# Kernel tuning notes

Hardware: AMD Instinct MI355X
Metric: run time of the kernel (lower is better)

Reference implementation:

```python
import jax, jax.numpy as jnp
import numpy as np

N = 100000   # nodes
E = 400000   # edges (avg degree 4, NoC-mesh-like)
H = 512      # hidden_channels
F_IN = 1     # num_node_features


def _lin(key, fan_in, fan_out):
    # torch.nn.Linear default init: U(-1/sqrt(fan_in), 1/sqrt(fan_in))
    bound = 1.0 / np.sqrt(fan_in)
    return jax.random.uniform(key, (fan_in, fan_out), jnp.float32, -bound, bound)


def setup_inputs() -> dict:
    key = jax.random.key(0)
    ks = jax.random.split(key, 16)
    inp = {
        "x": jax.random.normal(ks[0], (N, F_IN), jnp.float32),
        "edge_index": jax.random.randint(ks[1], (2, E), 0, N, jnp.int32),
        # conv1: in=1 -> out=512
        "w_rel1": _lin(ks[2], F_IN, H),
        "b_rel1": jax.random.uniform(ks[3], (H,), jnp.float32, -1.0, 1.0),
        "w_root1": _lin(ks[4], F_IN, H),
        # conv2..4: 512 -> 512
        "w_rel2": _lin(ks[5], H, H),
        "b_rel2": jax.random.uniform(ks[6], (H,), jnp.float32, -1/np.sqrt(H), 1/np.sqrt(H)),
        "w_root2": _lin(ks[7], H, H),
        "w_rel3": _lin(ks[8], H, H),
        "b_rel3": jax.random.uniform(ks[9], (H,), jnp.float32, -1/np.sqrt(H), 1/np.sqrt(H)),
        "w_root3": _lin(ks[10], H, H),
        "w_rel4": _lin(ks[11], H, H),
        "b_rel4": jax.random.uniform(ks[12], (H,), jnp.float32, -1/np.sqrt(H), 1/np.sqrt(H)),
        "w_root4": _lin(ks[13], H, H),
    }
    return inp


def _graph_conv(x, src, dst, w_rel, b_rel, w_root):
    # PyG GraphConv (aggr='add'): out_i = W_rel @ sum_{j in N(i)} x_j + b_rel + W_root @ x_i
    # messages flow src (edge_index[0]) -> dst (edge_index[1])
    agg = jax.ops.segment_sum(x[src], dst, num_segments=N)  # [N, F_in]
    return agg @ w_rel + b_rel + x @ w_root


def reference(x, edge_index,
              w_rel1, b_rel1, w_root1,
              w_rel2, b_rel2, w_root2,
              w_rel3, b_rel3, w_root3,
              w_rel4, b_rel4, w_root4):
    src, dst = edge_index[0], edge_index[1]
    x1 = jax.nn.relu(_graph_conv(x,  src, dst, w_rel1, b_rel1, w_root1))
    x2 = jax.nn.relu(_graph_conv(x1, src, dst, w_rel2, b_rel2, w_root2)) + x1
    x3 = _graph_conv(x2, src, dst, w_rel3, b_rel3, w_root3) + x2
    x4 = _graph_conv(x3, src, dst, w_rel4, b_rel4, w_root4) + x3
    return x4
```

## Files before the change

### kernel.cpp

```cpp
#include <hip/hip_runtime.h>

#define NN 100000
#define EE 400000
#define HH 512
#define NB_SCAN 98

typedef __attribute__((ext_vector_type(8))) short short8;
typedef __attribute__((ext_vector_type(8))) unsigned short ushort8;
typedef __attribute__((ext_vector_type(4))) float f32x4;

__device__ inline unsigned short f2b(float f) {
    unsigned int u = __float_as_uint(f);
    return (unsigned short)((u + 0x7fffu + ((u >> 16) & 1u)) >> 16);
}
__device__ inline float b2f(unsigned short b) {
    return __uint_as_float(((unsigned int)b) << 16);
}

__global__ void histo_deg(const int* __restrict__ dst, int* __restrict__ deg) {
    int e = blockIdx.x * blockDim.x + threadIdx.x;
    if (e < EE) atomicAdd(&deg[dst[e]], 1);
}

__global__ void scan_reduce(const int* __restrict__ deg, int* __restrict__ blockSums) {
    __shared__ int s[256];
    int b = blockIdx.x, t = threadIdx.x;
    int base = b * 1024 + t * 4;
    int v = 0;
    #pragma unroll
    for (int j = 0; j < 4; ++j) { int i = base + j; if (i < NN) v += deg[i]; }
    s[t] = v; __syncthreads();
    for (int off = 128; off > 0; off >>= 1) {
        if (t < off) s[t] += s[t + off];
        __syncthreads();
    }
    if (t == 0) blockSums[b] = s[0];
}

__global__ void scan_top(int* __restrict__ blockSums, int* __restrict__ start) {
    __shared__ int s[128];
    int t = threadIdx.x;
    s[t] = (t < NB_SCAN) ? blockSums[t] : 0;
    __syncthreads();
    for (int off = 1; off < 128; off <<= 1) {
        int u = (t >= off) ? s[t - off] : 0;
        __syncthreads();
        s[t] += u;
        __syncthreads();
    }
    if (t < NB_SCAN) blockSums[t] = (t == 0) ? 0 : s[t - 1];
    if (t == 0) start[NN] = EE;
}

__global__ void scan_down(const int* __restrict__ deg, const int* __restrict__ blockSums,
                          int* __restrict__ start, int* __restrict__ cursor) {
    __shared__ int s[256];
    int b = blockIdx.x, t = threadIdx.x;
    int base = b * 1024 + t * 4;
    int v[4]; int sum = 0;
    #pragma unroll
    for (int j = 0; j < 4; ++j) {
        int i = base + j;
        v[j] = (i < NN) ? deg[i] : 0;
        sum += v[j];
    }
    s[t] = sum; __syncthreads();
    for (int off = 1; off < 256; off <<= 1) {
        int u = (t >= off) ? s[t - off] : 0;
        __syncthreads();
        s[t] += u;
        __syncthreads();
    }
    int excl = blockSums[b] + ((t == 0) ? 0 : s[t - 1]);
    #pragma unroll
    for (int j = 0; j < 4; ++j) {
        int i = base + j;
        if (i < NN) { start[i] = excl; cursor[i] = excl; excl += v[j]; }
    }
}

__global__ void csr_fill(const int* __restrict__ src, const int* __restrict__ dst,
                         int* __restrict__ cursor, int* __restrict__ eidx) {
    int e = blockIdx.x * blockDim.x + threadIdx.x;
    if (e < EE) {
        int p = atomicAdd(&cursor[dst[e]], 1);
        eidx[p] = src[e];
    }
}

__global__ void w_transpose_all(
    const float* __restrict__ w0, const float* __restrict__ w1,
    const float* __restrict__ w2, const float* __restrict__ w3,
    const float* __restrict__ w4, const float* __restrict__ w5,
    unsigned short* __restrict__ wt)
{
    int m = blockIdx.x >> 10;
    int idx = ((blockIdx.x & 1023) << 8) + threadIdx.x;
    int n = idx >> 9, k = idx & 511;
    const float* w = (m == 0) ? w0 : (m == 1) ? w1 : (m == 2) ? w2
                   : (m == 3) ? w3 : (m == 4) ? w4 : w5;
    wt[(size_t)m * 262144 + idx] = f2b(w[(size_t)k * HH + n]);
}

__global__ __launch_bounds__(256) void gather_rows_b(
    const unsigned short* __restrict__ xb, const int* __restrict__ start,
    const int* __restrict__ eidx, unsigned short* __restrict__ agg)
{
    int node = blockIdx.x * 4 + (threadIdx.x >> 6);
    if (node >= NN) return;
    int c0 = (threadIdx.x & 63) << 3;
    float a[8] = {0.f,0.f,0.f,0.f,0.f,0.f,0.f,0.f};
    int e0 = start[node], e1 = start[node + 1];
    int e = e0;
    for (; e + 4 <= e1; e += 4) {
        int s0 = eidx[e], s1 = eidx[e + 1], s2 = eidx[e + 2], s3 = eidx[e + 3];
        ushort8 v0 = *(const ushort8*)(xb + (size_t)s0 * HH + c0);
        ushort8 v1 = *(const ushort8*)(xb + (size_t)s1 * HH + c0);
        ushort8 v2 = *(const ushort8*)(xb + (size_t)s2 * HH + c0);
        ushort8 v3 = *(const ushort8*)(xb + (size_t)s3 * HH + c0);
        #pragma unroll
        for (int j = 0; j < 8; ++j)
            a[j] += (b2f(v0[j]) + b2f(v1[j])) + (b2f(v2[j]) + b2f(v3[j]));
    }
    for (; e < e1; ++e) {
        ushort8 v = *(const ushort8*)(xb + (size_t)eidx[e] * HH + c0);
        #pragma unroll
        for (int j = 0; j < 8; ++j) a[j] += b2f(v[j]);
    }
    ushort8 o;
    #pragma unroll
    for (int j = 0; j < 8; ++j) o[j] = f2b(a[j]);
    *(ushort8*)(agg + (size_t)node * HH + c0) = o;
}

__global__ void gather_scalar(const float* __restrict__ x, const int* __restrict__ start,
                              const int* __restrict__ eidx, float* __restrict__ agg0) {
    int i = blockIdx.x * blockDim.x + threadIdx.x;
    if (i >= NN) return;
    float s = 0.f;
    int e1 = start[i + 1];
    for (int e = start[i]; e < e1; ++e) s += x[eidx[e]];
    agg0[i] = s;
}

__global__ void layer1_expand(const float* __restrict__ x,
                              const float* __restrict__ agg0,
                              const float* __restrict__ w_rel,
                              const float* __restrict__ b,
                              const float* __restrict__ w_root,
                              unsigned short* __restrict__ x1b) {
    int idx = blockIdx.x * blockDim.x + threadIdx.x;
    int i = idx >> 7;
    if (i >= NN) return;
    int q = (idx & 127) << 2;
    float a = agg0[i], xv = x[i];
    float4 wr = *(const float4*)&w_rel[q];
    float4 bb = *(const float4*)&b[q];
    float4 wt = *(const float4*)&w_root[q];
    float4 o;
    o.x = fmaxf(fmaf(a, wr.x, fmaf(xv, wt.x, bb.x)), 0.f);
    o.y = fmaxf(fmaf(a, wr.y, fmaf(xv, wt.y, bb.y)), 0.f);
    o.z = fmaxf(fmaf(a, wr.z, fmaf(xv, wt.z, bb.z)), 0.f);
    o.w = fmaxf(fmaf(a, wr.w, fmaf(xv, wt.w, bb.w)), 0.f);
    ushort4 ob = { f2b(o.x), f2b(o.y), f2b(o.z), f2b(o.w) };
    *(ushort4*)&x1b[(size_t)i * HH + q] = ob;
}

__device__ inline void gload16(const void* g, void* l) {
    __builtin_amdgcn_global_load_lds(
        (const __attribute__((address_space(1))) unsigned int*)g,
        (__attribute__((address_space(3))) unsigned int*)l,
        16, 0, 0);
}

template<bool RELU, bool F32OUT>
__global__ __launch_bounds__(256, 3) void gemm_mfma(
    const unsigned short* __restrict__ AB, const unsigned short* __restrict__ XBp,
    const unsigned short* __restrict__ WrT, const unsigned short* __restrict__ WoT,
    const float* __restrict__ bias, const unsigned short* __restrict__ residb,
    float* __restrict__ out, unsigned short* __restrict__ outb)
{
    __shared__ unsigned short As[2 * 128 * 32];
    __shared__ unsigned short Bs[2 * 128 * 32];
    const int tid  = threadIdx.x;
    const int wave = tid >> 6, lane = tid & 63;

    const int bid = blockIdx.x;
    const int nid = (bid & 7) * 391 + (bid >> 3);
    const int col0 = (nid & 3) << 7;
    const int row0 = (nid >> 2) << 7;

    const int wr = wave >> 1, wc = wave & 1;
    const int l16 = lane & 15, lq = lane >> 4;
    const int sRow = lane >> 2;
    const int sColSwz = (((lane & 3) ^ ((lane >> 3) & 3)) << 3);
    const int xorslot = ((lq ^ ((lane >> 1) & 3)) << 3);

    int rowA[2], colB[2];
    #pragma unroll
    for (int i = 0; i < 2; ++i) {
        int chunk = (wave << 1) + i;
        int gr = row0 + chunk * 16 + sRow;
        rowA[i] = (gr >= NN) ? (NN - 1) : gr;
        colB[i] = col0 + chunk * 16 + sRow;
    }

    f32x4 acc[4][4];
    #pragma unroll
    for (int m = 0; m < 4; ++m)
        #pragma unroll
        for (int n = 0; n < 4; ++n) acc[m][n] = (f32x4){0.f,0.f,0.f,0.f};

    auto STAGE = [&](unsigned short* Asb, unsigned short* Bsb, int t) {
        const int k0 = t << 5;
        const unsigned short* Ap = (k0 < 512) ? AB  : XBp;
        const unsigned short* Wp = (k0 < 512) ? WrT : WoT;
        const int kk = k0 & 511;
        #pragma unroll
        for (int i = 0; i < 2; ++i) {
            int chunk = (wave << 1) + i;
            gload16(Ap + (size_t)rowA[i] * HH + kk + sColSwz, Asb + chunk * 512);
            gload16(Wp + (size_t)colB[i] * HH + kk + sColSwz, Bsb + chunk * 512);
        }
    };
    auto COMPUTE = [&](const unsigned short* Asb, const unsigned short* Bsb) {
        short8 af[4], bfv[4];
        #pragma unroll
        for (int m = 0; m < 4; ++m)
            af[m] = *(const short8*)(Asb + (wr * 64 + m * 16 + l16) * 32 + xorslot);
        #pragma unroll
        for (int n = 0; n < 4; ++n)
            bfv[n] = *(const short8*)(Bsb + (wc * 64 + n * 16 + l16) * 32 + xorslot);
        #pragma unroll
        for (int m = 0; m < 4; ++m)
            #pragma unroll
            for (int n = 0; n < 4; ++n)
                acc[m][n] = __builtin_amdgcn_mfma_f32_16x16x32_bf16(af[m], bfv[n], acc[m][n], 0, 0, 0);
    };

    unsigned short *A0 = As, *A1 = As + 4096, *B0 = Bs, *B1 = Bs + 4096;
    STAGE(A0, B0, 0);
    __syncthreads();
    #pragma unroll 1
    for (int t = 0; t < 32; t += 2) {
        STAGE(A1, B1, t + 1);
        COMPUTE(A0, B0);
        __syncthreads();
        if (t + 2 < 32) STAGE(A0, B0, t + 2);
        COMPUTE(A1, B1);
        __syncthreads();
    }

    float bias_n[4];
    #pragma unroll
    for (int n = 0; n < 4; ++n) bias_n[n] = bias[col0 + wc * 64 + n * 16 + l16];

    #pragma unroll
    for (int m = 0; m < 4; ++m) {
        #pragma unroll
        for (int j = 0; j < 4; ++j) {
            int row = row0 + wr * 64 + m * 16 + lq * 4 + j;
            if (row >= NN) continue;
            #pragma unroll
            for (int n = 0; n < 4; ++n) {
                int col = col0 + wc * 64 + n * 16 + l16;
                size_t off = (size_t)row * HH + col;
                float v = acc[m][n][j] + bias_n[n];
                if (RELU) v = fmaxf(v, 0.f);
                v += b2f(residb[off]);
                if (F32OUT) out[off] = v;
                else        outb[off] = f2b(v);
            }
        }
    }
}

extern "C" void kernel_launch(void* const* d_in, const int* in_sizes, int n_in,
                              void* d_out, int out_size, void* d_ws, size_t ws_size,
                              hipStream_t stream) {
    const float* x   = (const float*)d_in[0];
    const int*   ei  = (const int*)d_in[1];
    const int*   src = ei;
    const int*   dst = ei + EE;
    const float* w_rel1  = (const float*)d_in[2];
    const float* b_rel1  = (const float*)d_in[3];
    const float* w_root1 = (const float*)d_in[4];
    const float* w_rel2  = (const float*)d_in[5];
    const float* b_rel2  = (const float*)d_in[6];
    const float* w_root2 = (const float*)d_in[7];
    const float* w_rel3  = (const float*)d_in[8];
    const float* b_rel3  = (const float*)d_in[9];
    const float* w_root3 = (const float*)d_in[10];
    const float* w_rel4  = (const float*)d_in[11];
    const float* b_rel4  = (const float*)d_in[12];
    const float* w_root4 = (const float*)d_in[13];

    const size_t NH = (size_t)NN * HH;
    unsigned short* XB   = (unsigned short*)d_ws;
    unsigned short* XB2  = XB + NH;
    unsigned short* X3B  = XB2 + NH;
    unsigned short* AGB  = X3B + NH;
    unsigned short* WT   = AGB + NH;
    float*          agg0 = (float*)(WT + 6 * 262144);
    int*            csr  = (int*)(agg0 + NN);
    int* deg       = csr;
    int* start     = csr + NN;
    int* cursor    = start + NN + 1;
    int* eidx      = cursor + NN;
    int* blockSums = eidx + EE;
    float* out = (float*)d_out;

    unsigned short* WrT2 = WT;
    unsigned short* WoT2 = WT + 1 * 262144;
    unsigned short* WrT3 = WT + 2 * 262144;
    unsigned short* WoT3 = WT + 3 * 262144;
    unsigned short* WrT4 = WT + 4 * 262144;
    unsigned short* WoT4 = WT + 5 * 262144;

    const int gGemm = 3128;

    hipMemsetAsync(deg, 0, NN * sizeof(int), stream);
    histo_deg<<<(EE + 255) / 256, 256, 0, stream>>>(dst, deg);
    scan_reduce<<<NB_SCAN, 256, 0, stream>>>(deg, blockSums);
    scan_top<<<1, 128, 0, stream>>>(blockSums, start);
    scan_down<<<NB_SCAN, 256, 0, stream>>>(deg, blockSums, start, cursor);
    csr_fill<<<(EE + 255) / 256, 256, 0, stream>>>(src, dst, cursor, eidx);

    w_transpose_all<<<6144, 256, 0, stream>>>(
        w_rel2, w_root2, w_rel3, w_root3, w_rel4, w_root4, WT);

    gather_scalar<<<(NN + 255) / 256, 256, 0, stream>>>(x, start, eidx, agg0);
    layer1_expand<<<50000, 256, 0, stream>>>(x, agg0, w_rel1, b_rel1, w_root1, XB);

    gather_rows_b<<<25000, 256, 0, stream>>>(XB, start, eidx, AGB);
    gemm_mfma<true, false><<<gGemm, 256, 0, stream>>>(
        AGB, XB, WrT2, WoT2, b_rel2, XB, nullptr, XB2);

    gather_rows_b<<<25000, 256, 0, stream>>>(XB2, start, eidx, AGB);
    gemm_mfma<false, false><<<gGemm, 256, 0, stream>>>(
        AGB, XB2, WrT3, WoT3, b_rel3, XB2, nullptr, X3B);

    gather_rows_b<<<25000, 256, 0, stream>>>(X3B, start, eidx, AGB);
    gemm_mfma<false, true><<<gGemm, 256, 0, stream>>>(
        AGB, X3B, WrT4, WoT4, b_rel4, X3B, out, nullptr);
}
```

Measured before the change: 802.0 us.

## Store aggregated features and transposed weights in pre-tiled swizzled GEMM layout

The gather kernel now writes aggregated rows, and the weight transpose writes weights, straight into a 128x32 tile-blocked layout with an XOR swizzle that matches the GEMM's LDS arrangement. The GEMM stage can then load each tile as one contiguous block, using lane-linear 16-byte loads instead of strided per-row addresses. This is meant to improve global load coalescing and cut address arithmetic in the GEMM. In exchange, the gather kernel's stores become scattered rather than row-contiguous, and the aggregation buffer is padded to a multiple of 128 rows.

```diff
diff --git a/kernel.cpp b/kernel.cpp
--- a/kernel.cpp
+++ b/kernel.cpp
@@ -99,7 +99,9 @@
     int n = idx >> 9, k = idx & 511;
     const float* w = (m == 0) ? w0 : (m == 1) ? w1 : (m == 2) ? w2
                    : (m == 3) ? w3 : (m == 4) ? w4 : w5;
-    wt[(size_t)m * 262144 + idx] = f2b(w[(size_t)k * HH + n]);
+    size_t pos = ((size_t)(n >> 7) << 16) + (((k >> 5) & 15) << 12) + ((n & 127) << 5)
+               + (((((k >> 3) & 3) ^ ((n >> 1) & 3))) << 3) + (k & 7);
+    wt[(size_t)m * 262144 + pos] = f2b(w[(size_t)k * HH + n]);
 }
 
 __global__ __launch_bounds__(256) void gather_rows_b(
@@ -108,7 +110,8 @@
 {
     int node = blockIdx.x * 4 + (threadIdx.x >> 6);
     if (node >= NN) return;
-    int c0 = (threadIdx.x & 63) << 3;
+    int l = threadIdx.x & 63;
+    int c0 = l << 3;
     float a[8] = {0.f,0.f,0.f,0.f,0.f,0.f,0.f,0.f};
     int e0 = start[node], e1 = start[node + 1];
     int e = e0;
@@ -130,7 +133,10 @@
     ushort8 o;
     #pragma unroll
     for (int j = 0; j < 8; ++j) o[j] = f2b(a[j]);
-    *(ushort8*)(agg + (size_t)node * HH + c0) = o;
+    size_t pa = ((size_t)(node >> 7) << 16) + ((size_t)(l >> 2) << 12)
+              + ((size_t)(node & 127) << 5)
+              + ((size_t)(((l & 3) ^ ((node >> 1) & 3)) << 3));
+    *(ushort8*)(agg + pa) = o;
 }
 
 __global__ void gather_scalar(const float* __restrict__ x, const int* __restrict__ start,
@@ -189,6 +195,8 @@
     const int nid = (bid & 7) * 391 + (bid >> 3);
     const int col0 = (nid & 3) << 7;
     const int row0 = (nid >> 2) << 7;
+    const int rb = nid >> 2;
+    const int cb = nid & 3;
 
     const int wr = wave >> 1, wc = wave & 1;
     const int l16 = lane & 15, lq = lane >> 4;
@@ -196,13 +204,12 @@
     const int sColSwz = (((lane & 3) ^ ((lane >> 3) & 3)) << 3);
     const int xorslot = ((lq ^ ((lane >> 1) & 3)) << 3);
 
-    int rowA[2], colB[2];
+    int rowA[2];
     #pragma unroll
     for (int i = 0; i < 2; ++i) {
         int chunk = (wave << 1) + i;
         int gr = row0 + chunk * 16 + sRow;
         rowA[i] = (gr >= NN) ? (NN - 1) : gr;
-        colB[i] = col0 + chunk * 16 + sRow;
     }
 
     f32x4 acc[4][4];
@@ -212,15 +219,30 @@
         for (int n = 0; n < 4; ++n) acc[m][n] = (f32x4){0.f,0.f,0.f,0.f};
 
     auto STAGE = [&](unsigned short* Asb, unsigned short* Bsb, int t) {
-        const int k0 = t << 5;
-        const unsigned short* Ap = (k0 < 512) ? AB  : XBp;
-        const unsigned short* Wp = (k0 < 512) ? WrT : WoT;
-        const int kk = k0 & 511;
-        #pragma unroll
-        for (int i = 0; i < 2; ++i) {
-            int chunk = (wave << 1) + i;
-            gload16(Ap + (size_t)rowA[i] * HH + kk + sColSwz, Asb + chunk * 512);
-            gload16(Wp + (size_t)colB[i] * HH + kk + sColSwz, Bsb + chunk * 512);
+        const int c = t & 15;
+        {
+            const unsigned short* Wp = (t < 16) ? WrT : WoT;
+            const unsigned short* srcB = Wp + ((size_t)cb << 16) + (c << 12);
+            #pragma unroll
+            for (int i = 0; i < 2; ++i) {
+                int j = (wave << 1) + i;
+                gload16(srcB + (j << 9) + (lane << 3), Bsb + (j << 9));
+            }
+        }
+        if (t < 16) {
+            const unsigned short* srcA = AB + ((size_t)rb << 16) + (c << 12);
+            #pragma unroll
+            for (int i = 0; i < 2; ++i) {
+                int j = (wave << 1) + i;
+                gload16(srcA + (j << 9) + (lane << 3), Asb + (j << 9));
+            }
+        } else {
+            const int kk = c << 5;
+            #pragma unroll
+            for (int i = 0; i < 2; ++i) {
+                int chunk = (wave << 1) + i;
+                gload16(XBp + (size_t)rowA[i] * HH + kk + sColSwz, Asb + chunk * 512);
+            }
         }
     };
     auto COMPUTE = [&](const unsigned short* Asb, const unsigned short* Bsb) {
@@ -295,12 +317,13 @@
     const float* b_rel4  = (const float*)d_in[12];
     const float* w_root4 = (const float*)d_in[13];
 
-    const size_t NH = (size_t)NN * HH;
+    const size_t NH  = (size_t)NN * HH;
+    const size_t NHP = (size_t)100096 * HH;
     unsigned short* XB   = (unsigned short*)d_ws;
     unsigned short* XB2  = XB + NH;
     unsigned short* X3B  = XB2 + NH;
     unsigned short* AGB  = X3B + NH;
-    unsigned short* WT   = AGB + NH;
+    unsigned short* WT   = AGB + NHP;
     float*          agg0 = (float*)(WT + 6 * 262144);
     int*            csr  = (int*)(agg0 + NN);
     int* deg       = csr;
```

New measurement: 762.3 us (median of 3 runs). -5.0%, faster.

## Store bf16 activations and weights in pre-tiled swizzled layout for contiguous GEMM staging

Applied to the files above, without the earlier changes.

Introduces a tiled layout (128-row by 32-column blocks, with an XOR swizzle already applied) for all bf16 activation buffers and transposed weights. The GEMM's global-to-LDS loads become fully contiguous 4KB tile copies with no per-lane row address computation or row clamping. Buffers are padded to a multiple of 128 rows. The gather kernel now reads 16-byte pieces from scattered tile locations rather than contiguous 1KB rows, which may reduce coalescing in the aggregation step.

```diff
diff --git a/kernel.cpp b/kernel.cpp
--- a/kernel.cpp
+++ b/kernel.cpp
@@ -15,6 +15,13 @@
 }
 __device__ inline float b2f(unsigned short b) {
     return __uint_as_float(((unsigned int)b) << 16);
+}
+
+__device__ inline size_t pidx(int row, int col) {
+    return ((size_t)(row >> 7) << 16) + ((size_t)(col >> 5) << 12)
+         + ((size_t)(row & 127) << 5)
+         + ((size_t)((((col >> 3) & 3) ^ ((row >> 1) & 3)) << 3))
+         + (size_t)(col & 7);
 }
 
 __global__ void histo_deg(const int* __restrict__ dst, int* __restrict__ deg) {
@@ -99,7 +106,7 @@
     int n = idx >> 9, k = idx & 511;
     const float* w = (m == 0) ? w0 : (m == 1) ? w1 : (m == 2) ? w2
                    : (m == 3) ? w3 : (m == 4) ? w4 : w5;
-    wt[(size_t)m * 262144 + idx] = f2b(w[(size_t)k * HH + n]);
+    wt[(size_t)m * 262144 + pidx(n, k)] = f2b(w[(size_t)k * HH + n]);
 }
 
 __global__ __launch_bounds__(256) void gather_rows_b(
@@ -108,29 +115,30 @@
 {
     int node = blockIdx.x * 4 + (threadIdx.x >> 6);
     if (node >= NN) return;
-    int c0 = (threadIdx.x & 63) << 3;
+    int l = threadIdx.x & 63;
+    int c0 = l << 3;
     float a[8] = {0.f,0.f,0.f,0.f,0.f,0.f,0.f,0.f};
     int e0 = start[node], e1 = start[node + 1];
     int e = e0;
     for (; e + 4 <= e1; e += 4) {
         int s0 = eidx[e], s1 = eidx[e + 1], s2 = eidx[e + 2], s3 = eidx[e + 3];
-        ushort8 v0 = *(const ushort8*)(xb + (size_t)s0 * HH + c0);
-        ushort8 v1 = *(const ushort8*)(xb + (size_t)s1 * HH + c0);
-        ushort8 v2 = *(const ushort8*)(xb + (size_t)s2 * HH + c0);
-        ushort8 v3 = *(const ushort8*)(xb + (size_t)s3 * HH + c0);
+        ushort8 v0 = *(const ushort8*)(xb + pidx(s0, c0));
+        ushort8 v1 = *(const ushort8*)(xb + pidx(s1, c0));
+        ushort8 v2 = *(const ushort8*)(xb + pidx(s2, c0));
+        ushort8 v3 = *(const ushort8*)(xb + pidx(s3, c0));
         #pragma unroll
         for (int j = 0; j < 8; ++j)
             a[j] += (b2f(v0[j]) + b2f(v1[j])) + (b2f(v2[j]) + b2f(v3[j]));
     }
     for (; e < e1; ++e) {
-        ushort8 v = *(const ushort8*)(xb + (size_t)eidx[e] * HH + c0);
+        ushort8 v = *(const ushort8*)(xb + pidx(eidx[e], c0));
         #pragma unroll
         for (int j = 0; j < 8; ++j) a[j] += b2f(v[j]);
     }
     ushort8 o;
     #pragma unroll
     for (int j = 0; j < 8; ++j) o[j] = f2b(a[j]);
-    *(ushort8*)(agg + (size_t)node * HH + c0) = o;
+    *(ushort8*)(agg + pidx(node, c0)) = o;
 }
 
 __global__ void gather_scalar(const float* __restrict__ x, const int* __restrict__ start,
@@ -163,7 +171,7 @@
     o.z = fmaxf(fmaf(a, wr.z, fmaf(xv, wt.z, bb.z)), 0.f);
     o.w = fmaxf(fmaf(a, wr.w, fmaf(xv, wt.w, bb.w)), 0.f);
     ushort4 ob = { f2b(o.x), f2b(o.y), f2b(o.z), f2b(o.w) };
-    *(ushort4*)&x1b[(size_t)i * HH + q] = ob;
+    *(ushort4*)&x1b[pidx(i, q)] = ob;
 }
 
 __device__ inline void gload16(const void* g, void* l) {
@@ -189,22 +197,13 @@
     const int nid = (bid & 7) * 391 + (bid >> 3);
     const int col0 = (nid & 3) << 7;
     const int row0 = (nid >> 2) << 7;
+    const int rb = nid >> 2;
+    const int cb = nid & 3;
 
     const int wr = wave >> 1, wc = wave & 1;
     const int l16 = lane & 15, lq = lane >> 4;
-    const int sRow = lane >> 2;
-    const int sColSwz = (((lane & 3) ^ ((lane >> 3) & 3)) << 3);
     const int xorslot = ((lq ^ ((lane >> 1) & 3)) << 3);
 
-    int rowA[2], colB[2];
-    #pragma unroll
-    for (int i = 0; i < 2; ++i) {
-        int chunk = (wave << 1) + i;
-        int gr = row0 + chunk * 16 + sRow;
-        rowA[i] = (gr >= NN) ? (NN - 1) : gr;
-        colB[i] = col0 + chunk * 16 + sRow;
-    }
-
     f32x4 acc[4][4];
     #pragma unroll
     for (int m = 0; m < 4; ++m)
@@ -212,15 +211,14 @@
         for (int n = 0; n < 4; ++n) acc[m][n] = (f32x4){0.f,0.f,0.f,0.f};
 
     auto STAGE = [&](unsigned short* Asb, unsigned short* Bsb, int t) {
-        const int k0 = t << 5;
-        const unsigned short* Ap = (k0 < 512) ? AB  : XBp;
-        const unsigned short* Wp = (k0 < 512) ? WrT : WoT;
-        const int kk = k0 & 511;
+        const int c = t & 15;
+        const unsigned short* srcA = ((t < 16) ? AB  : XBp) + ((size_t)rb << 16) + (c << 12);
+        const unsigned short* srcB = ((t < 16) ? WrT : WoT) + ((size_t)cb << 16) + (c << 12);
         #pragma unroll
         for (int i = 0; i < 2; ++i) {
-            int chunk = (wave << 1) + i;
-            gload16(Ap + (size_t)rowA[i] * HH + kk + sColSwz, Asb + chunk * 512);
-            gload16(Wp + (size_t)colB[i] * HH + kk + sColSwz, Bsb + chunk * 512);
+            int j = (wave << 1) + i;
+            gload16(srcA + (j << 9) + (lane << 3), Asb + (j << 9));
+            gload16(srcB + (j << 9) + (lane << 3), Bsb + (j << 9));
         }
     };
     auto COMPUTE = [&](const unsigned short* Asb, const unsigned short* Bsb) {
@@ -230,7 +228,7 @@
             af[m] = *(const short8*)(Asb + (wr * 64 + m * 16 + l16) * 32 + xorslot);
         #pragma unroll
         for (int n = 0; n < 4; ++n)
-            bfv[n] = *(const short8*)(Bsb + (wc * 64 + n * 16 + l16) * 32 + xorslot);
+            bfv[n] = *(const short8*)(Bs + (Bsb - Bs) + (wc * 64 + n * 16 + l16) * 32 + xorslot);
         #pragma unroll
         for (int m = 0; m < 4; ++m)
             #pragma unroll
@@ -264,12 +262,12 @@
             #pragma unroll
             for (int n = 0; n < 4; ++n) {
                 int col = col0 + wc * 64 + n * 16 + l16;
-                size_t off = (size_t)row * HH + col;
                 float v = acc[m][n][j] + bias_n[n];
                 if (RELU) v = fmaxf(v, 0.f);
-                v += b2f(residb[off]);
-                if (F32OUT) out[off] = v;
-                else        outb[off] = f2b(v);
+                size_t po = pidx(row, col);
+                v += b2f(residb[po]);
+                if (F32OUT) out[(size_t)row * HH + col] = v;
+                else        outb[po] = f2b(v);
             }
         }
     }
@@ -295,12 +293,12 @@
     const float* b_rel4  = (const float*)d_in[12];
     const float* w_root4 = (const float*)d_in[13];
 
-    const size_t NH = (size_t)NN * HH;
+    const size_t NHP = (size_t)100096 * HH;
     unsigned short* XB   = (unsigned short*)d_ws;
-    unsigned short* XB2  = XB + NH;
-    unsigned short* X3B  = XB2 + NH;
-    unsigned short* AGB  = X3B + NH;
-    unsigned short* WT   = AGB + NH;
+    unsigned short* XB2  = XB + NHP;
+    unsigned short* X3B  = XB2 + NHP;
+    unsigned short* AGB  = X3B + NHP;
+    unsigned short* WT   = AGB + NHP;
     float*          agg0 = (float*)(WT + 6 * 262144);
     int*            csr  = (int*)(agg0 + NN);
     int* deg       = csr;
```

After: 985.2 us. +22.8%, slower.
